# Kernel tuning notes

Hardware: AMD Instinct MI355X
Metric: run time of the kernel (lower is better)

## Reference

```python
import jax, jax.numpy as jnp
import numpy as np
from jax import lax

B, N, C, H = 8, 1024, 384, 6
D = C // H
SCALE = D ** -0.5
EPS = 1e-5


def setup_inputs() -> dict:
    key = jax.random.key(0)
    ks = jax.random.split(key, 10)
    s = 0.02
    return {
        "x": jax.random.normal(ks[0], (B, N, C), jnp.float32),
        "w_qkv": jax.random.normal(ks[1], (3 * C, C), jnp.float32) * s,
        "w_proj": jax.random.normal(ks[2], (C, C), jnp.float32) * s,
        "b_proj": jax.random.normal(ks[3], (C,), jnp.float32) * s,
        "w_kq": jax.random.normal(ks[4], (H, 1, 3, 3), jnp.float32) * 0.1,   # depthwise (groups=H)
        "b_kq": jax.random.normal(ks[5], (H,), jnp.float32) * 0.1,
        "w_head": jax.random.normal(ks[6], (H, H, 1, 1), jnp.float32) * 0.1,  # 1x1 head-mixing conv
        "b_head": jax.random.normal(ks[7], (H,), jnp.float32) * 0.1,
        "gn_w": jnp.ones((H,), jnp.float32),
        "gn_b": jnp.zeros((H,), jnp.float32),
    }


def reference(x, w_qkv, w_proj, b_proj, w_kq, b_kq, w_head, b_head, gn_w, gn_b):
    # qkv projection (torch Linear: y = x @ W.T)
    qkv = (x @ w_qkv.T).reshape(B, N, 3, H, D).transpose(2, 0, 3, 1, 4)  # [3,B,H,N,D]
    q, k, v = qkv[0], qkv[1], qkv[2]

    # attention logits [B,H,N,N]
    logits = jnp.einsum("bhnd,bhmd->bhnm", q, k) * SCALE

    # depthwise (groups=H) 3x3 conv over the NxN logit map
    logits = lax.conv_general_dilated(
        logits, w_kq, window_strides=(1, 1), padding=((1, 1), (1, 1)),
        dimension_numbers=("NCHW", "OIHW", "NCHW"), feature_group_count=H,
    ) + b_kq[None, :, None, None]

    attn = jax.nn.softmax(logits, axis=-1)

    # 1x1 conv mixing heads
    attn = jnp.einsum("oh,bhnm->bonm", w_head[:, :, 0, 0], attn) + b_head[None, :, None, None]

    # GroupNorm(num_groups=H, channels=H): per (b, head) stats over NxN
    mean = attn.mean(axis=(2, 3), keepdims=True)
    var = ((attn - mean) ** 2).mean(axis=(2, 3), keepdims=True)
    attn = (attn - mean) * lax.rsqrt(var + EPS)
    attn = attn * gn_w[None, :, None, None] + gn_b[None, :, None, None]

    out = jnp.einsum("bhnm,bhmd->bhnd", attn, v)
    out = out.transpose(0, 2, 1, 3).reshape(B, N, C)
    return out @ w_proj.T + b_proj
```

## Files before the change

### kernel.cpp

```cpp
#include <hip/hip_runtime.h>

typedef unsigned short u16;
typedef __attribute__((ext_vector_type(8))) short short8;
typedef __attribute__((ext_vector_type(4))) float f32x4;

#define MFMA(a, b, c) __builtin_amdgcn_mfma_f32_16x16x32_bf16((a), (b), (c), 0, 0, 0)

__device__ inline float bf2f(u16 u) {
  union { unsigned int i; float f; } w; w.i = ((unsigned int)u) << 16; return w.f;
}
__device__ inline u16 f2bf(float x) {
  union { float f; unsigned int i; } u; u.f = x;
  unsigned int r = u.i + 0x7fffu + ((u.i >> 16) & 1u);
  return (u16)(r >> 16);
}
__device__ inline unsigned int pk2(float a, float b) {
  return (unsigned int)f2bf(a) | ((unsigned int)f2bf(b) << 16);
}
__device__ inline void unpack8(uint4 v, float* f) {
  union { unsigned int i; float g; } c;
  c.i = v.x << 16;          f[0] = c.g;
  c.i = v.x & 0xffff0000u;  f[1] = c.g;
  c.i = v.y << 16;          f[2] = c.g;
  c.i = v.y & 0xffff0000u;  f[3] = c.g;
  c.i = v.z << 16;          f[4] = c.g;
  c.i = v.z & 0xffff0000u;  f[5] = c.g;
  c.i = v.w << 16;          f[6] = c.g;
  c.i = v.w & 0xffff0000u;  f[7] = c.g;
}

static const size_t SZ_QKV = (size_t)48 * 1024 * 64 * 2;
static const size_t SZ_MAP = (size_t)48 * 1024 * 1024 * 2;
static const size_t OFF_Q  = 0;
static const size_t OFF_K  = OFF_Q + SZ_QKV;
static const size_t OFF_VT = OFF_K + SZ_QKV;
static const size_t OFF_S  = OFF_VT + SZ_QKV;
static const size_t OFF_QM = OFF_S + SZ_MAP;
static const size_t OFF_OT = OFF_QM + SZ_MAP;
static const size_t OFF_ST = OFF_OT + SZ_QKV;
static const size_t OFF_CS = OFF_ST + 896;
static const size_t OFF_AD = OFF_CS + 12288;
static const size_t OFF_AL = OFF_AD + 12288;

__global__ __launch_bounds__(256) void k_qkv(const float* __restrict__ x,
                                             const float* __restrict__ w,
                                             u16* __restrict__ qb,
                                             u16* __restrict__ kb,
                                             u16* __restrict__ vT) {
  __shared__ u16 As[128 * 64];
  __shared__ u16 Bs[128 * 64];
  const int t = threadIdx.x;
  const int m0 = blockIdx.x * 128;
  const int n0 = blockIdx.y * 128;
  const int wave = t >> 6, lane = t & 63;
  const int wm = (wave & 1) * 64, wn = (wave >> 1) * 64;
  const int fr = lane & 15;
  const int fk = (lane >> 4) * 8;
  f32x4 acc[4][4] = {};
  for (int k0 = 0; k0 < 384; k0 += 64) {
#pragma unroll
    for (int i = 0; i < 4; ++i) {
      int e = (i * 256 + t) * 8;
      int row = e >> 6, col = e & 63;
      const float* xp = &x[(size_t)(m0 + row) * 384 + k0 + col];
      const float* wp = &w[(size_t)(n0 + row) * 384 + k0 + col];
      float4 a0 = *(const float4*)xp, a1 = *(const float4*)(xp + 4);
      uint4 av; av.x = pk2(a0.x, a0.y); av.y = pk2(a0.z, a0.w);
      av.z = pk2(a1.x, a1.y); av.w = pk2(a1.z, a1.w);
      *(uint4*)&As[e] = av;
      float4 b0 = *(const float4*)wp, b1 = *(const float4*)(wp + 4);
      uint4 bv; bv.x = pk2(b0.x, b0.y); bv.y = pk2(b0.z, b0.w);
      bv.z = pk2(b1.x, b1.y); bv.w = pk2(b1.z, b1.w);
      *(uint4*)&Bs[e] = bv;
    }
    __syncthreads();
#pragma unroll
    for (int ks = 0; ks < 2; ++ks) {
      const int ko = ks * 32 + fk;
      short8 a[4], b[4];
#pragma unroll
      for (int mi = 0; mi < 4; ++mi) a[mi] = *(const short8*)&As[(wm + mi * 16 + fr) * 64 + ko];
#pragma unroll
      for (int ni = 0; ni < 4; ++ni) b[ni] = *(const short8*)&Bs[(wn + ni * 16 + fr) * 64 + ko];
#pragma unroll
      for (int mi = 0; mi < 4; ++mi)
#pragma unroll
        for (int ni = 0; ni < 4; ++ni) acc[mi][ni] = MFMA(a[mi], b[ni], acc[mi][ni]);
    }
    __syncthreads();
  }
#pragma unroll
  for (int mi = 0; mi < 4; ++mi) {
#pragma unroll
    for (int ni = 0; ni < 4; ++ni) {
      int gc = n0 + wn + ni * 16 + fr;
      int s = gc / 384;
      int rem = gc - s * 384;
      int h = rem >> 6, d = rem & 63;
#pragma unroll
      for (int r = 0; r < 4; ++r) {
        int gm = m0 + wm + mi * 16 + (lane >> 4) * 4 + r;
        int b_ = gm >> 10, n = gm & 1023;
        u16 val = f2bf(acc[mi][ni][r]);
        size_t base = (size_t)(b_ * 6 + h) << 16;
        if (s == 0)      qb[base + (size_t)n * 64 + d] = val;
        else if (s == 1) kb[base + (size_t)n * 64 + d] = val;
        else             vT[base + (size_t)d * 1024 + n] = val;
      }
    }
  }
}

__global__ __launch_bounds__(256) void k_qk(const u16* __restrict__ qb,
                                            const u16* __restrict__ kb,
                                            u16* __restrict__ S) {
  __shared__ u16 As[128 * 64];
  __shared__ u16 Bs[128 * 64];
  const int t = threadIdx.x;
  const int m0 = blockIdx.x * 128, n0 = blockIdx.y * 128;
  const int bh = blockIdx.z;
  const u16* A = qb + ((size_t)bh << 16);
  const u16* Bp = kb + ((size_t)bh << 16);
  const int wave = t >> 6, lane = t & 63;
  const int wm = (wave & 1) * 64, wn = (wave >> 1) * 64;
  const int fr = lane & 15;
  const int fk = (lane >> 4) * 8;
  f32x4 acc[4][4] = {};
#pragma unroll
  for (int i = 0; i < 4; ++i) {
    int e = (i * 256 + t) * 8;
    *(uint4*)&As[e] = *(const uint4*)&A[(size_t)m0 * 64 + e];
    *(uint4*)&Bs[e] = *(const uint4*)&Bp[(size_t)n0 * 64 + e];
  }
  __syncthreads();
#pragma unroll
  for (int ks = 0; ks < 2; ++ks) {
    const int ko = ks * 32 + fk;
    short8 a[4], b[4];
#pragma unroll
    for (int mi = 0; mi < 4; ++mi) a[mi] = *(const short8*)&As[(wm + mi * 16 + fr) * 64 + ko];
#pragma unroll
    for (int ni = 0; ni < 4; ++ni) b[ni] = *(const short8*)&Bs[(wn + ni * 16 + fr) * 64 + ko];
#pragma unroll
    for (int mi = 0; mi < 4; ++mi)
#pragma unroll
      for (int ni = 0; ni < 4; ++ni) acc[mi][ni] = MFMA(a[mi], b[ni], acc[mi][ni]);
  }
  const size_t sb = (size_t)bh << 20;
#pragma unroll
  for (int mi = 0; mi < 4; ++mi)
#pragma unroll
    for (int ni = 0; ni < 4; ++ni) {
      int gc = n0 + wn + ni * 16 + fr;
#pragma unroll
      for (int r = 0; r < 4; ++r) {
        int gm = m0 + wm + mi * 16 + (lane >> 4) * 4 + r;
        S[sb + (size_t)gm * 1024 + gc] = f2bf(acc[mi][ni][r] * 0.125f);
      }
    }
}

__global__ __launch_bounds__(256) void k_conv_softmax(const u16* __restrict__ S,
                                                      const float* __restrict__ w_kq,
                                                      u16* __restrict__ Qb) {
  __shared__ u16 Sr[10 * 1040];
  __shared__ float red[4];
  const int t = threadIdx.x;
  const int bh = blockIdx.y;
  const int h = bh % 6;
  const int r0 = blockIdx.x * 8;
  const u16* Sp = S + ((size_t)bh << 20);
  float wv[9];
#pragma unroll
  for (int i = 0; i < 9; ++i) wv[i] = w_kq[h * 9 + i];
  if (t < 10) { Sr[t * 1040 + 7] = 0; Sr[t * 1040 + 1032] = 0; }
#pragma unroll
  for (int c = 0; c < 5; ++c) {
    int e = (c * 256 + t) * 8;
    int i = e >> 10, col = e & 1023;
    int g = r0 - 1 + i;
    uint4 val = make_uint4(0u, 0u, 0u, 0u);
    if (g >= 0 && g < 1024) val = *(const uint4*)&Sp[(size_t)g * 1024 + col];
    *(uint4*)&Sr[i * 1040 + 8 + col] = val;
  }
  __syncthreads();
  const int half = t >> 7;
  const int lane = t & 63;
  const int m0 = (t & 127) * 8;
  for (int pass = 0; pass < 4; ++pass) {
    int rr = pass * 2 + half;
    float o8[8];
#pragma unroll
    for (int j = 0; j < 8; ++j) o8[j] = 0.f;
#pragma unroll
    for (int i = 0; i < 3; ++i) {
      const u16* rowp = &Sr[(rr + i) * 1040 + 8];
      float left = bf2f(rowp[m0 - 1]);
      float md[8];
      unpack8(*(const uint4*)&rowp[m0], md);
      float right = bf2f(rowp[m0 + 8]);
      float w0 = wv[i * 3 + 0], w1 = wv[i * 3 + 1], w2 = wv[i * 3 + 2];
      o8[0] += w0 * left + w1 * md[0] + w2 * md[1];
#pragma unroll
      for (int j = 1; j < 7; ++j) o8[j] += w0 * md[j - 1] + w1 * md[j] + w2 * md[j + 1];
      o8[7] += w0 * md[6] + w1 * md[7] + w2 * right;
    }
    float mx = o8[0];
#pragma unroll
    for (int j = 1; j < 8; ++j) mx = fmaxf(mx, o8[j]);
    for (int off = 32; off; off >>= 1) mx = fmaxf(mx, __shfl_xor(mx, off, 64));
    if (lane == 0) red[t >> 6] = mx;
    __syncthreads();
    float rmax = fmaxf(red[half * 2], red[half * 2 + 1]);
    __syncthreads();
    float e8[8], s = 0.f;
#pragma unroll
    for (int j = 0; j < 8; ++j) { e8[j] = __expf(o8[j] - rmax); s += e8[j]; }
    for (int off = 32; off; off >>= 1) s += __shfl_xor(s, off, 64);
    if (lane == 0) red[t >> 6] = s;
    __syncthreads();
    float rsum = red[half * 2] + red[half * 2 + 1];
    __syncthreads();
    float scale = 1024.f / rsum;
    unsigned int pk[4];
#pragma unroll
    for (int jj = 0; jj < 4; ++jj)
      pk[jj] = pk2(e8[2 * jj] * scale - 1.f, e8[2 * jj + 1] * scale - 1.f);
    int n = r0 + rr;
    *(uint4*)&Qb[((size_t)bh << 20) + (size_t)n * 1024 + m0] = make_uint4(pk[0], pk[1], pk[2], pk[3]);
  }
}

__global__ __launch_bounds__(256) void k_gram(const u16* __restrict__ Qm,
                                              float* __restrict__ gstats) {
  __shared__ float red[4][27];
  const int t = threadIdx.x;
  const int n0 = blockIdx.x * 8;
  const int b_ = blockIdx.y;
  const size_t qbase = ((size_t)(b_ * 6)) << 20;
  uint4 buf[4][6];
#pragma unroll
  for (int p = 0; p < 4; ++p) {
    int e = (p * 256 + t) * 8;
    int row = e >> 10, m = e & 1023;
#pragma unroll
    for (int hh = 0; hh < 6; ++hh)
      buf[p][hh] = *(const uint4*)&Qm[qbase + (((size_t)hh) << 20) + (size_t)(n0 + row) * 1024 + m];
  }
  float s[6] = {0.f, 0.f, 0.f, 0.f, 0.f, 0.f};
  float G[21];
#pragma unroll
  for (int i = 0; i < 21; ++i) G[i] = 0.f;
#pragma unroll
  for (int p = 0; p < 4; ++p) {
    float qf[6][8];
#pragma unroll
    for (int hh = 0; hh < 6; ++hh) unpack8(buf[p][hh], qf[hh]);
#pragma unroll
    for (int j = 0; j < 8; ++j) {
      int idx = 0;
#pragma unroll
      for (int h1 = 0; h1 < 6; ++h1) {
        s[h1] += qf[h1][j];
#pragma unroll
        for (int h2 = h1; h2 < 6; ++h2) { G[idx] += qf[h1][j] * qf[h2][j]; ++idx; }
      }
    }
  }
  const int wave = t >> 6, lane = t & 63;
#pragma unroll
  for (int i = 0; i < 6; ++i) {
    float v = s[i];
    for (int off = 32; off; off >>= 1) v += __shfl_xor(v, off, 64);
    if (lane == 0) red[wave][i] = v;
  }
#pragma unroll
  for (int i = 0; i < 21; ++i) {
    float v = G[i];
    for (int off = 32; off; off >>= 1) v += __shfl_xor(v, off, 64);
    if (lane == 0) red[wave][6 + i] = v;
  }
  __syncthreads();
  if (t < 27)
    atomicAdd(&gstats[b_ * 27 + t], red[0][t] + red[1][t] + red[2][t] + red[3][t]);
}

__global__ __launch_bounds__(256) void k_colsum(const u16* __restrict__ vT,
                                                float* __restrict__ colsum) {
  __shared__ float acc[64];
  const int t = threadIdx.x;
  const int bh = blockIdx.x;
  if (t < 64) acc[t] = 0.f;
  __syncthreads();
  const int lane = t & 63;
  for (int c = 0; c < 32; ++c) {
    size_t l = (size_t)c * 2048 + (size_t)t * 8;
    uint4 u = *(const uint4*)&vT[((size_t)bh << 16) + l];
    float f[8];
    unpack8(u, f);
    float part = f[0] + f[1] + f[2] + f[3] + f[4] + f[5] + f[6] + f[7];
    for (int off = 32; off; off >>= 1) part += __shfl_xor(part, off, 64);
    if (lane == 0) atomicAdd(&acc[(int)(l >> 10)], part);
  }
  __syncthreads();
  if (t < 64) colsum[bh * 64 + t] = acc[t];
}

__global__ __launch_bounds__(256) void k_finalize(const float* __restrict__ gstats,
                                                  const float* __restrict__ colsum,
                                                  const float* __restrict__ wh,
                                                  const float* __restrict__ gn_w,
                                                  const float* __restrict__ gn_b,
                                                  float* __restrict__ addend,
                                                  float* __restrict__ alphaArr) {
  int gid = blockIdx.x * 256 + threadIdx.x;
  int bo = gid >> 6, d = gid & 63;
  int b_ = bo / 6, o = bo - b_ * 6;
  const float* g = &gstats[b_ * 27];
  float w[6];
#pragma unroll
  for (int hh = 0; hh < 6; ++hh) w[hh] = wh[o * 6 + hh];
  float s1 = 0.f;
#pragma unroll
  for (int hh = 0; hh < 6; ++hh) s1 += w[hh] * g[hh];
  float s2 = 0.f;
  int idx = 6;
#pragma unroll
  for (int h1 = 0; h1 < 6; ++h1)
#pragma unroll
    for (int h2 = h1; h2 < 6; ++h2) {
      float c = g[idx]; ++idx;
      s2 += (h1 == h2 ? w[h1] * w[h1] : 2.f * w[h1] * w[h2]) * c;
    }
  const float inv = 1.f / 1048576.f;
  float mu = s1 * inv;
  float var = s2 * inv - mu * mu;
  float alpha = gn_w[o] * rsqrtf(var + 1e-5f * 1048576.f);
  float beta = gn_b[o] - alpha * mu;
  addend[gid] = beta * colsum[gid];
  if (d == 0) alphaArr[bo] = alpha;
}

__global__ __launch_bounds__(256) void k_pvmix(const u16* __restrict__ Qm,
                                               const u16* __restrict__ vT,
                                               const float* __restrict__ wh,
                                               const float* __restrict__ alphaArr,
                                               const float* __restrict__ addend,
                                               u16* __restrict__ otmp) {
  __shared__ u16 Am[64 * 72];
  __shared__ u16 Vm[64 * 72];
  const int t = threadIdx.x;
  const int n0 = blockIdx.x * 64;
  const int bo = blockIdx.y;
  const int b_ = bo / 6, o = bo - b_ * 6;
  const int wave = t >> 6, lane = t & 63;
  const int fr = lane & 15, quad = lane >> 4;
  float wo[6];
#pragma unroll
  for (int hh = 0; hh < 6; ++hh) wo[hh] = wh[o * 6 + hh];
  const size_t qbase = ((size_t)(b_ * 6)) << 20;
  const u16* vp = vT + ((size_t)bo << 16);
  f32x4 acc[4] = {};
  for (int mc = 0; mc < 16; ++mc) {
    const int mbase = mc * 64;
#pragma unroll
    for (int i = 0; i < 2; ++i) {
      int it = i * 256 + t;
      int row = it >> 3, mg = it & 7;
      int m = mbase + mg * 8;
      float mix[8] = {0.f, 0.f, 0.f, 0.f, 0.f, 0.f, 0.f, 0.f};
#pragma unroll
      for (int hh = 0; hh < 6; ++hh) {
        float qf[8];
        unpack8(*(const uint4*)&Qm[qbase + (((size_t)hh) << 20) + (size_t)(n0 + row) * 1024 + m], qf);
        float w = wo[hh];
#pragma unroll
        for (int j = 0; j < 8; ++j) mix[j] += w * qf[j];
      }
      uint4 pk4;
      pk4.x = pk2(mix[0], mix[1]); pk4.y = pk2(mix[2], mix[3]);
      pk4.z = pk2(mix[4], mix[5]); pk4.w = pk2(mix[6], mix[7]);
      *(uint4*)&Am[row * 72 + mg * 8] = pk4;
    }
#pragma unroll
    for (int i = 0; i < 2; ++i) {
      int it = i * 256 + t;
      int d = it >> 3, mg = it & 7;
      *(uint4*)&Vm[d * 72 + mg * 8] = *(const uint4*)&vp[(size_t)d * 1024 + mbase + mg * 8];
    }
    __syncthreads();
#pragma unroll
    for (int ks = 0; ks < 2; ++ks) {
      short8 a = *(const short8*)&Am[(wave * 16 + fr) * 72 + ks * 32 + quad * 8];
#pragma unroll
      for (int ni = 0; ni < 4; ++ni) {
        short8 b = *(const short8*)&Vm[(ni * 16 + fr) * 72 + ks * 32 + quad * 8];
        acc[ni] = MFMA(a, b, acc[ni]);
      }
    }
    __syncthreads();
  }
  const float alpha = alphaArr[bo];
#pragma unroll
  for (int ni = 0; ni < 4; ++ni) {
    int d = ni * 16 + fr;
    float add = addend[bo * 64 + d];
#pragma unroll
    for (int r = 0; r < 4; ++r) {
      int n = n0 + wave * 16 + quad * 4 + r;
      otmp[((size_t)(b_ * 1024 + n)) * 384 + o * 64 + d] = f2bf(acc[ni][r] * alpha + add);
    }
  }
}

__global__ __launch_bounds__(256) void k_proj(const u16* __restrict__ A,
                                              const float* __restrict__ w,
                                              const float* __restrict__ bias,
                                              float* __restrict__ out) {
  __shared__ u16 As[128 * 64];
  __shared__ u16 Bs[128 * 64];
  const int t = threadIdx.x;
  const int m0 = blockIdx.x * 128;
  const int n0 = blockIdx.y * 128;
  const int wave = t >> 6, lane = t & 63;
  const int wm = (wave & 1) * 64, wn = (wave >> 1) * 64;
  const int fr = lane & 15;
  const int fk = (lane >> 4) * 8;
  f32x4 acc[4][4] = {};
  for (int k0 = 0; k0 < 384; k0 += 64) {
#pragma unroll
    for (int i = 0; i < 4; ++i) {
      int e = (i * 256 + t) * 8;
      int row = e >> 6, col = e & 63;
      *(uint4*)&As[e] = *(const uint4*)&A[(size_t)(m0 + row) * 384 + k0 + col];
      const float* wp = &w[(size_t)(n0 + row) * 384 + k0 + col];
      float4 b0 = *(const float4*)wp, b1 = *(const float4*)(wp + 4);
      uint4 bv; bv.x = pk2(b0.x, b0.y); bv.y = pk2(b0.z, b0.w);
      bv.z = pk2(b1.x, b1.y); bv.w = pk2(b1.z, b1.w);
      *(uint4*)&Bs[e] = bv;
    }
    __syncthreads();
#pragma unroll
    for (int ks = 0; ks < 2; ++ks) {
      const int ko = ks * 32 + fk;
      short8 a[4], b[4];
#pragma unroll
      for (int mi = 0; mi < 4; ++mi) a[mi] = *(const short8*)&As[(wm + mi * 16 + fr) * 64 + ko];
#pragma unroll
      for (int ni = 0; ni < 4; ++ni) b[ni] = *(const short8*)&Bs[(wn + ni * 16 + fr) * 64 + ko];
#pragma unroll
      for (int mi = 0; mi < 4; ++mi)
#pragma unroll
        for (int ni = 0; ni < 4; ++ni) acc[mi][ni] = MFMA(a[mi], b[ni], acc[mi][ni]);
    }
    __syncthreads();
  }
#pragma unroll
  for (int mi = 0; mi < 4; ++mi)
#pragma unroll
    for (int ni = 0; ni < 4; ++ni) {
      int gc = n0 + wn + ni * 16 + fr;
      float bv = bias[gc];
#pragma unroll
      for (int r = 0; r < 4; ++r) {
        int gm = m0 + wm + mi * 16 + (lane >> 4) * 4 + r;
        out[(size_t)gm * 384 + gc] = acc[mi][ni][r] + bv;
      }
    }
}

extern "C" void kernel_launch(void* const* d_in, const int* in_sizes, int n_in,
                              void* d_out, int out_size, void* d_ws, size_t ws_size,
                              hipStream_t stream) {
  (void)in_sizes; (void)n_in; (void)out_size; (void)ws_size;
  const float* x      = (const float*)d_in[0];
  const float* w_qkv  = (const float*)d_in[1];
  const float* w_proj = (const float*)d_in[2];
  const float* b_proj = (const float*)d_in[3];
  const float* w_kq   = (const float*)d_in[4];
  const float* w_head = (const float*)d_in[6];
  const float* gn_w   = (const float*)d_in[8];
  const float* gn_b   = (const float*)d_in[9];

  char* ws = (char*)d_ws;
  u16*   qb      = (u16*)(ws + OFF_Q);
  u16*   kb      = (u16*)(ws + OFF_K);
  u16*   vT      = (u16*)(ws + OFF_VT);
  u16*   Sb      = (u16*)(ws + OFF_S);
  u16*   Qm      = (u16*)(ws + OFF_QM);
  u16*   otmp    = (u16*)(ws + OFF_OT);
  float* gstats  = (float*)(ws + OFF_ST);
  float* colsum  = (float*)(ws + OFF_CS);
  float* addend  = (float*)(ws + OFF_AD);
  float* alphaA  = (float*)(ws + OFF_AL);

  hipMemsetAsync(gstats, 0, 896, stream);
  k_qkv<<<dim3(64, 9), 256, 0, stream>>>(x, w_qkv, qb, kb, vT);
  k_qk<<<dim3(8, 8, 48), 256, 0, stream>>>(qb, kb, Sb);
  k_conv_softmax<<<dim3(128, 48), 256, 0, stream>>>(Sb, w_kq, Qm);
  k_gram<<<dim3(128, 8), 256, 0, stream>>>(Qm, gstats);
  k_colsum<<<dim3(48), 256, 0, stream>>>(vT, colsum);
  k_finalize<<<dim3(12), 256, 0, stream>>>(gstats, colsum, w_head, gn_w, gn_b, addend, alphaA);
  k_pvmix<<<dim3(16, 48), 256, 0, stream>>>(Qm, vT, w_head, alphaA, addend, otmp);
  k_proj<<<dim3(64, 3), 256, 0, stream>>>(otmp, w_proj, b_proj, (float*)d_out);
}
```

Baseline: 329.2 us.

## Fuse GroupNorm stats into pvmix, split K across two blocks, apply affine after

Drops the separate gram kernel, which re-read the whole 6-head attention map to build head Gram statistics. The GroupNorm sum and sum of squares are now accumulated directly from the mixed values inside the PV kernel. The PV kernel is split in two along the key dimension for more parallelism, with register prefetch of the next Q/V tile. Unnormalized partial results go to fp32 buffers, and a new elementwise kernel applies alpha and beta afterwards. The cost is extra fp32 intermediate traffic, one more launch, and stats taken from fp32 mixes rather than the exact bf16 values fed to the MFMA.

After: 316.1 us. 1.04x faster.

```diff
diff --git a/kernel.cpp b/kernel.cpp
--- a/kernel.cpp
+++ b/kernel.cpp
@@ -35,6 +35,8 @@
 static const size_t OFF_K  = OFF_Q + SZ_QKV;
 static const size_t OFF_VT = OFF_K + SZ_QKV;
 static const size_t OFF_S  = OFF_VT + SZ_QKV;
+static const size_t OFF_U0 = OFF_S;
+static const size_t OFF_U1 = OFF_S + 12582912;
 static const size_t OFF_QM = OFF_S + SZ_MAP;
 static const size_t OFF_OT = OFF_QM + SZ_MAP;
 static const size_t OFF_ST = OFF_OT + SZ_QKV;
@@ -231,60 +233,6 @@
   }
 }
 
-__global__ __launch_bounds__(256) void k_gram(const u16* __restrict__ Qm,
-                                              float* __restrict__ gstats) {
-  __shared__ float red[4][27];
-  const int t = threadIdx.x;
-  const int n0 = blockIdx.x * 8;
-  const int b_ = blockIdx.y;
-  const size_t qbase = ((size_t)(b_ * 6)) << 20;
-  uint4 buf[4][6];
-#pragma unroll
-  for (int p = 0; p < 4; ++p) {
-    int e = (p * 256 + t) * 8;
-    int row = e >> 10, m = e & 1023;
-#pragma unroll
-    for (int hh = 0; hh < 6; ++hh)
-      buf[p][hh] = *(const uint4*)&Qm[qbase + (((size_t)hh) << 20) + (size_t)(n0 + row) * 1024 + m];
-  }
-  float s[6] = {0.f, 0.f, 0.f, 0.f, 0.f, 0.f};
-  float G[21];
-#pragma unroll
-  for (int i = 0; i < 21; ++i) G[i] = 0.f;
-#pragma unroll
-  for (int p = 0; p < 4; ++p) {
-    float qf[6][8];
-#pragma unroll
-    for (int hh = 0; hh < 6; ++hh) unpack8(buf[p][hh], qf[hh]);
-#pragma unroll
-    for (int j = 0; j < 8; ++j) {
-      int idx = 0;
-#pragma unroll
-      for (int h1 = 0; h1 < 6; ++h1) {
-        s[h1] += qf[h1][j];
-#pragma unroll
-        for (int h2 = h1; h2 < 6; ++h2) { G[idx] += qf[h1][j] * qf[h2][j]; ++idx; }
-      }
-    }
-  }
-  const int wave = t >> 6, lane = t & 63;
-#pragma unroll
-  for (int i = 0; i < 6; ++i) {
-    float v = s[i];
-    for (int off = 32; off; off >>= 1) v += __shfl_xor(v, off, 64);
-    if (lane == 0) red[wave][i] = v;
-  }
-#pragma unroll
-  for (int i = 0; i < 21; ++i) {
-    float v = G[i];
-    for (int off = 32; off; off >>= 1) v += __shfl_xor(v, off, 64);
-    if (lane == 0) red[wave][6 + i] = v;
-  }
-  __syncthreads();
-  if (t < 27)
-    atomicAdd(&gstats[b_ * 27 + t], red[0][t] + red[1][t] + red[2][t] + red[3][t]);
-}
-
 __global__ __launch_bounds__(256) void k_colsum(const u16* __restrict__ vT,
                                                 float* __restrict__ colsum) {
   __shared__ float acc[64];
@@ -306,32 +254,117 @@
   if (t < 64) colsum[bh * 64 + t] = acc[t];
 }
 
-__global__ __launch_bounds__(256) void k_finalize(const float* __restrict__ gstats,
+__global__ __launch_bounds__(256) void k_pvmix(const u16* __restrict__ Qm,
+                                               const u16* __restrict__ vT,
+                                               const float* __restrict__ wh,
+                                               float* __restrict__ U0,
+                                               float* __restrict__ U1,
+                                               float* __restrict__ stats) {
+  __shared__ u16 Am[64 * 72];
+  __shared__ u16 Vm[64 * 72];
+  const int t = threadIdx.x;
+  const int n0 = blockIdx.x * 64;
+  const int bo = blockIdx.y;
+  const int mh = blockIdx.z;
+  const int b_ = bo / 6, o = bo - b_ * 6;
+  const int wave = t >> 6, lane = t & 63;
+  const int fr = lane & 15, quad = lane >> 4;
+  const int srow = t >> 3, smg8 = (t & 7) * 8;
+  float wo[6];
+#pragma unroll
+  for (int hh = 0; hh < 6; ++hh) wo[hh] = wh[o * 6 + hh];
+  const size_t qbase = ((size_t)(b_ * 6)) << 20;
+  const u16* vp = vT + ((size_t)bo << 16);
+  const int mstart = mh * 512;
+  uint4 qpre[2][6];
+  uint4 vpre[2];
+  {
+    const int m = mstart + smg8;
+#pragma unroll
+    for (int i = 0; i < 2; ++i)
+#pragma unroll
+      for (int hh = 0; hh < 6; ++hh)
+        qpre[i][hh] = *(const uint4*)&Qm[qbase + (((size_t)hh) << 20) +
+                                         (size_t)(n0 + i * 32 + srow) * 1024 + m];
+    vpre[0] = *(const uint4*)&vp[(size_t)srow * 1024 + m];
+    vpre[1] = *(const uint4*)&vp[(size_t)(32 + srow) * 1024 + m];
+  }
+  f32x4 acc[4] = {};
+  float s1 = 0.f, s2 = 0.f;
+  for (int mc = 0; mc < 8; ++mc) {
+    __syncthreads();
+#pragma unroll
+    for (int i = 0; i < 2; ++i) {
+      float mix[8] = {0.f, 0.f, 0.f, 0.f, 0.f, 0.f, 0.f, 0.f};
+#pragma unroll
+      for (int hh = 0; hh < 6; ++hh) {
+        float qf[8];
+        unpack8(qpre[i][hh], qf);
+        float w = wo[hh];
+#pragma unroll
+        for (int j = 0; j < 8; ++j) mix[j] += w * qf[j];
+      }
+#pragma unroll
+      for (int j = 0; j < 8; ++j) { s1 += mix[j]; s2 += mix[j] * mix[j]; }
+      uint4 pk4;
+      pk4.x = pk2(mix[0], mix[1]); pk4.y = pk2(mix[2], mix[3]);
+      pk4.z = pk2(mix[4], mix[5]); pk4.w = pk2(mix[6], mix[7]);
+      *(uint4*)&Am[(i * 32 + srow) * 72 + smg8] = pk4;
+    }
+    *(uint4*)&Vm[srow * 72 + smg8] = vpre[0];
+    *(uint4*)&Vm[(32 + srow) * 72 + smg8] = vpre[1];
+    if (mc < 7) {
+      const int m = mstart + (mc + 1) * 64 + smg8;
+#pragma unroll
+      for (int i = 0; i < 2; ++i)
+#pragma unroll
+        for (int hh = 0; hh < 6; ++hh)
+          qpre[i][hh] = *(const uint4*)&Qm[qbase + (((size_t)hh) << 20) +
+                                           (size_t)(n0 + i * 32 + srow) * 1024 + m];
+      vpre[0] = *(const uint4*)&vp[(size_t)srow * 1024 + m];
+      vpre[1] = *(const uint4*)&vp[(size_t)(32 + srow) * 1024 + m];
+    }
+    __syncthreads();
+#pragma unroll
+    for (int ks = 0; ks < 2; ++ks) {
+      short8 a = *(const short8*)&Am[(wave * 16 + fr) * 72 + ks * 32 + quad * 8];
+#pragma unroll
+      for (int ni = 0; ni < 4; ++ni) {
+        short8 b = *(const short8*)&Vm[(ni * 16 + fr) * 72 + ks * 32 + quad * 8];
+        acc[ni] = MFMA(a, b, acc[ni]);
+      }
+    }
+  }
+  float* Up = mh ? U1 : U0;
+#pragma unroll
+  for (int ni = 0; ni < 4; ++ni) {
+    int d = ni * 16 + fr;
+#pragma unroll
+    for (int r = 0; r < 4; ++r) {
+      int n = n0 + wave * 16 + quad * 4 + r;
+      Up[((size_t)(bo * 1024 + n)) * 64 + d] = acc[ni][r];
+    }
+  }
+  for (int off = 32; off; off >>= 1) {
+    s1 += __shfl_xor(s1, off, 64);
+    s2 += __shfl_xor(s2, off, 64);
+  }
+  if (lane == 0) {
+    atomicAdd(&stats[bo * 2 + 0], s1);
+    atomicAdd(&stats[bo * 2 + 1], s2);
+  }
+}
+
+__global__ __launch_bounds__(256) void k_finalize(const float* __restrict__ stats,
                                                   const float* __restrict__ colsum,
-                                                  const float* __restrict__ wh,
                                                   const float* __restrict__ gn_w,
                                                   const float* __restrict__ gn_b,
                                                   float* __restrict__ addend,
                                                   float* __restrict__ alphaArr) {
   int gid = blockIdx.x * 256 + threadIdx.x;
   int bo = gid >> 6, d = gid & 63;
-  int b_ = bo / 6, o = bo - b_ * 6;
-  const float* g = &gstats[b_ * 27];
-  float w[6];
-#pragma unroll
-  for (int hh = 0; hh < 6; ++hh) w[hh] = wh[o * 6 + hh];
-  float s1 = 0.f;
-#pragma unroll
-  for (int hh = 0; hh < 6; ++hh) s1 += w[hh] * g[hh];
-  float s2 = 0.f;
-  int idx = 6;
-#pragma unroll
-  for (int h1 = 0; h1 < 6; ++h1)
-#pragma unroll
-    for (int h2 = h1; h2 < 6; ++h2) {
-      float c = g[idx]; ++idx;
-      s2 += (h1 == h2 ? w[h1] * w[h1] : 2.f * w[h1] * w[h2]) * c;
-    }
+  int o = bo % 6;
+  float s1 = stats[bo * 2], s2 = stats[bo * 2 + 1];
   const float inv = 1.f / 1048576.f;
   float mu = s1 * inv;
   float var = s2 * inv - mu * mu;
@@ -341,76 +374,25 @@
   if (d == 0) alphaArr[bo] = alpha;
 }
 
-__global__ __launch_bounds__(256) void k_pvmix(const u16* __restrict__ Qm,
-                                               const u16* __restrict__ vT,
-                                               const float* __restrict__ wh,
+__global__ __launch_bounds__(256) void k_apply(const float* __restrict__ U0,
+                                               const float* __restrict__ U1,
                                                const float* __restrict__ alphaArr,
                                                const float* __restrict__ addend,
                                                u16* __restrict__ otmp) {
-  __shared__ u16 Am[64 * 72];
-  __shared__ u16 Vm[64 * 72];
-  const int t = threadIdx.x;
-  const int n0 = blockIdx.x * 64;
-  const int bo = blockIdx.y;
-  const int b_ = bo / 6, o = bo - b_ * 6;
-  const int wave = t >> 6, lane = t & 63;
-  const int fr = lane & 15, quad = lane >> 4;
-  float wo[6];
-#pragma unroll
-  for (int hh = 0; hh < 6; ++hh) wo[hh] = wh[o * 6 + hh];
-  const size_t qbase = ((size_t)(b_ * 6)) << 20;
-  const u16* vp = vT + ((size_t)bo << 16);
-  f32x4 acc[4] = {};
-  for (int mc = 0; mc < 16; ++mc) {
-    const int mbase = mc * 64;
-#pragma unroll
-    for (int i = 0; i < 2; ++i) {
-      int it = i * 256 + t;
-      int row = it >> 3, mg = it & 7;
-      int m = mbase + mg * 8;
-      float mix[8] = {0.f, 0.f, 0.f, 0.f, 0.f, 0.f, 0.f, 0.f};
-#pragma unroll
-      for (int hh = 0; hh < 6; ++hh) {
-        float qf[8];
-        unpack8(*(const uint4*)&Qm[qbase + (((size_t)hh) << 20) + (size_t)(n0 + row) * 1024 + m], qf);
-        float w = wo[hh];
-#pragma unroll
-        for (int j = 0; j < 8; ++j) mix[j] += w * qf[j];
-      }
-      uint4 pk4;
-      pk4.x = pk2(mix[0], mix[1]); pk4.y = pk2(mix[2], mix[3]);
-      pk4.z = pk2(mix[4], mix[5]); pk4.w = pk2(mix[6], mix[7]);
-      *(uint4*)&Am[row * 72 + mg * 8] = pk4;
-    }
-#pragma unroll
-    for (int i = 0; i < 2; ++i) {
-      int it = i * 256 + t;
-      int d = it >> 3, mg = it & 7;
-      *(uint4*)&Vm[d * 72 + mg * 8] = *(const uint4*)&vp[(size_t)d * 1024 + mbase + mg * 8];
-    }
-    __syncthreads();
-#pragma unroll
-    for (int ks = 0; ks < 2; ++ks) {
-      short8 a = *(const short8*)&Am[(wave * 16 + fr) * 72 + ks * 32 + quad * 8];
-#pragma unroll
-      for (int ni = 0; ni < 4; ++ni) {
-        short8 b = *(const short8*)&Vm[(ni * 16 + fr) * 72 + ks * 32 + quad * 8];
-        acc[ni] = MFMA(a, b, acc[ni]);
-      }
-    }
-    __syncthreads();
-  }
-  const float alpha = alphaArr[bo];
-#pragma unroll
-  for (int ni = 0; ni < 4; ++ni) {
-    int d = ni * 16 + fr;
-    float add = addend[bo * 64 + d];
-#pragma unroll
-    for (int r = 0; r < 4; ++r) {
-      int n = n0 + wave * 16 + quad * 4 + r;
-      otmp[((size_t)(b_ * 1024 + n)) * 384 + o * 64 + d] = f2bf(acc[ni][r] * alpha + add);
-    }
-  }
+  int i = blockIdx.x * 256 + threadIdx.x;
+  int e = i * 4;
+  int d4 = e & 63;
+  int n = (e >> 6) & 1023;
+  int bo = e >> 16;
+  float al = alphaArr[bo];
+  const float* ap = &addend[bo * 64 + d4];
+  float4 u0 = *(const float4*)&U0[e];
+  float4 u1 = *(const float4*)&U1[e];
+  int b = bo / 6, o = bo - b * 6;
+  uint2 w;
+  w.x = pk2(al * (u0.x + u1.x) + ap[0], al * (u0.y + u1.y) + ap[1]);
+  w.y = pk2(al * (u0.z + u1.z) + ap[2], al * (u0.w + u1.w) + ap[3]);
+  *(uint2*)&otmp[((size_t)(b * 1024 + n)) * 384 + o * 64 + d4] = w;
 }
 
 __global__ __launch_bounds__(256) void k_proj(const u16* __restrict__ A,
@@ -487,20 +469,22 @@
   u16*   kb      = (u16*)(ws + OFF_K);
   u16*   vT      = (u16*)(ws + OFF_VT);
   u16*   Sb      = (u16*)(ws + OFF_S);
+  float* U0      = (float*)(ws + OFF_U0);
+  float* U1      = (float*)(ws + OFF_U1);
   u16*   Qm      = (u16*)(ws + OFF_QM);
   u16*   otmp    = (u16*)(ws + OFF_OT);
-  float* gstats  = (float*)(ws + OFF_ST);
+  float* stats   = (float*)(ws + OFF_ST);
   float* colsum  = (float*)(ws + OFF_CS);
   float* addend  = (float*)(ws + OFF_AD);
   float* alphaA  = (float*)(ws + OFF_AL);
 
-  hipMemsetAsync(gstats, 0, 896, stream);
+  hipMemsetAsync(stats, 0, 512, stream);
   k_qkv<<<dim3(64, 9), 256, 0, stream>>>(x, w_qkv, qb, kb, vT);
   k_qk<<<dim3(8, 8, 48), 256, 0, stream>>>(qb, kb, Sb);
   k_conv_softmax<<<dim3(128, 48), 256, 0, stream>>>(Sb, w_kq, Qm);
-  k_gram<<<dim3(128, 8), 256, 0, stream>>>(Qm, gstats);
   k_colsum<<<dim3(48), 256, 0, stream>>>(vT, colsum);
-  k_finalize<<<dim3(12), 256, 0, stream>>>(gstats, colsum, w_head, gn_w, gn_b, addend, alphaA);
-  k_pvmix<<<dim3(16, 48), 256, 0, stream>>>(Qm, vT, w_head, alphaA, addend, otmp);
+  k_pvmix<<<dim3(16, 48, 2), 256, 0, stream>>>(Qm, vT, w_head, U0, U1, stats);
+  k_finalize<<<dim3(12), 256, 0, stream>>>(stats, colsum, gn_w, gn_b, addend, alphaA);
+  k_apply<<<dim3(3072), 256, 0, stream>>>(U0, U1, alphaA, addend, otmp);
   k_proj<<<dim3(64, 3), 256, 0, stream>>>(otmp, w_proj, b_proj, (float*)d_out);
 }
```
